# Optimization experiments

Hardware: AMD Instinct MI355X
Metric: run time of the kernel (lower is better)

The kernel has to match this reference:

```python
import jax, jax.numpy as jnp
import numpy as np

B, T, D, H = 4, 2048, 1024, 16
DH = D // H  # 64


def setup_inputs() -> dict:
    key = jax.random.key(0)
    ks = jax.random.split(key, 5)
    s = 0.02
    return {
        "x": jax.random.normal(ks[0], (B, T, D), dtype=jnp.float32),
        "Wq": jax.random.normal(ks[1], (D, D), dtype=jnp.float32) * s,
        "Wk": jax.random.normal(ks[2], (D, D), dtype=jnp.float32) * s,
        "Wv": jax.random.normal(ks[3], (D, D), dtype=jnp.float32) * s,
        "Wo": jax.random.normal(ks[4], (D, D), dtype=jnp.float32) * s,
        "bo": jnp.zeros((D,), dtype=jnp.float32),
    }


def reference(x, Wq, Wk, Wv, Wo, bo):
    b, t, d = x.shape
    # QKV projections (no bias, matching qkv_bias=False)
    q = (x @ Wq).reshape(b, t, H, DH).transpose(0, 2, 1, 3)  # [B,H,T,Dh]
    k = (x @ Wk).reshape(b, t, H, DH).transpose(0, 2, 1, 3)
    v = (x @ Wv).reshape(b, t, H, DH).transpose(0, 2, 1, 3)
    scores = jnp.einsum('bhqd,bhkd->bhqk', q, k)  # [B,H,T,T]
    # mask strictly-upper triangle (future positions) with -inf, then scale
    causal = jnp.triu(jnp.ones((t, t), dtype=bool), k=1)
    scores = jnp.where(causal[None, None], -jnp.inf, scores)
    attn = jax.nn.softmax(scores / np.float32(np.sqrt(DH)), axis=-1)
    ctx = jnp.einsum('bhqk,bhkd->bhqd', attn, v)  # [B,H,T,Dh]
    ctx = ctx.transpose(0, 2, 1, 3).reshape(b, t, d)
    return ctx @ Wo + bo
```

## Files before the change

kernel.cpp:

```cpp
#include <hip/hip_runtime.h>
#include <math.h>
#include <stdint.h>

typedef unsigned short u16;
typedef __bf16 bf16x8 __attribute__((ext_vector_type(8)));
typedef unsigned short u16x8 __attribute__((ext_vector_type(8)));
typedef float f32x4 __attribute__((ext_vector_type(4)));

constexpr int Tc = 2048, Dc = 1024, Hc = 16, Mc = 8192;
constexpr size_t NQKV = (size_t)Mc * Dc;
constexpr size_t NW = (size_t)Dc * Dc;

__device__ __forceinline__ u16 f2bf(float f) {
    union { float f; uint32_t u; } c; c.f = f;
    uint32_t u = c.u;
    u += 0x7FFFu + ((u >> 16) & 1u);
    return (u16)(u >> 16);
}

__device__ __forceinline__ bf16x8 ldbf8(const u16* p) {
    u16x8 v = *(const u16x8*)p;
    return __builtin_bit_cast(bf16x8, v);
}

__device__ __forceinline__ float fexp2(float x) {
#if __has_builtin(__builtin_amdgcn_exp2f)
    return __builtin_amdgcn_exp2f(x);
#else
    return exp2f(x);
#endif
}

__device__ __forceinline__ void gload_lds16(const void* g, void* l) {
    __builtin_amdgcn_global_load_lds(
        (__attribute__((address_space(1))) void*)(uintptr_t)g,
        (__attribute__((address_space(3))) void*)l, 16, 0, 0);
}

__global__ __launch_bounds__(256)
void cvt_x_kernel(const float* __restrict__ x, u16* __restrict__ xb)
{
    int i = blockIdx.x * 256 + threadIdx.x;
    float4 v = ((const float4*)x)[i];
    ushort4 o;
    o.x = f2bf(v.x); o.y = f2bf(v.y); o.z = f2bf(v.z); o.w = f2bf(v.w);
    ((ushort4*)xb)[i] = o;
}

__global__ __launch_bounds__(256)
void wt_cvt_kernel(const float* __restrict__ Wq, const float* __restrict__ Wk,
                   const float* __restrict__ Wv, const float* __restrict__ Wo,
                   u16* __restrict__ WTq, u16* __restrict__ WTk,
                   u16* __restrict__ WTv, u16* __restrict__ WTo)
{
    __shared__ float Ts[64][65];
    const int z = blockIdx.z;
    const float* W = (z == 0) ? Wq : (z == 1) ? Wk : (z == 2) ? Wv : Wo;
    u16* WT        = (z == 0) ? WTq : (z == 1) ? WTk : (z == 2) ? WTv : WTo;
    const int k0 = blockIdx.x * 64, n0 = blockIdx.y * 64;
    const int tid = threadIdx.x;
    #pragma unroll
    for (int it = 0; it < 16; ++it) {
        int flat = it * 256 + tid;
        int r = flat >> 6, c = flat & 63;
        Ts[r][c] = W[(size_t)(k0 + r) * Dc + n0 + c];
    }
    __syncthreads();
    #pragma unroll
    for (int it = 0; it < 16; ++it) {
        int flat = it * 256 + tid;
        int rn = flat >> 6, ck = flat & 63;
        WT[(size_t)(n0 + rn) * Dc + k0 + ck] = f2bf(Ts[ck][rn]);
    }
}

__global__ __launch_bounds__(256)
void qkv_gemm_kernel(const u16* __restrict__ xb,
                     const u16* __restrict__ WTq, const u16* __restrict__ WTk,
                     const u16* __restrict__ WTv,
                     u16* __restrict__ Qb, u16* __restrict__ Kb, u16* __restrict__ Vb)
{
    const int z = blockIdx.z;
    const u16* WT = (z == 0) ? WTq : (z == 1) ? WTk : WTv;
    u16* outp     = (z == 0) ? Qb  : (z == 1) ? Kb  : Vb;
    const float scale = (z == 0) ? 0.125f * 1.44269504088896f : 1.0f;

    __shared__ __align__(16) u16 As[128 * 32];
    __shared__ __align__(16) u16 Bs[128 * 32];

    const int tid = threadIdx.x, lane = tid & 63, w = tid >> 6;
    const int wm = w >> 1, wn = w & 1;
    const int m0 = blockIdx.x * 128, n0 = blockIdx.y * 128;

    f32x4 acc[4][4] = {};

    for (int k0 = 0; k0 < Dc; k0 += 32) {
        __syncthreads();
        #pragma unroll
        for (int t = 0; t < 2; ++t) {
            int ci = w * 64 + t * 256 + lane;
            int r = ci >> 2, p = ci & 3;
            int pc = p ^ ((r >> 1) & 3);
            gload_lds16(xb + (size_t)(m0 + r) * Dc + k0 + pc * 8,
                        As + (size_t)(w * 64 + t * 256) * 8);
            gload_lds16(WT + (size_t)(n0 + r) * Dc + k0 + pc * 8,
                        Bs + (size_t)(w * 64 + t * 256) * 8);
        }
        __syncthreads();

        bf16x8 a[4], b[4];
        #pragma unroll
        for (int i = 0; i < 4; ++i) {
            int row = wm * 64 + i * 16 + (lane & 15);
            a[i] = ldbf8(As + row * 32 + (((lane >> 4) ^ ((row >> 1) & 3)) * 8));
            int col = wn * 64 + i * 16 + (lane & 15);
            b[i] = ldbf8(Bs + col * 32 + (((lane >> 4) ^ ((col >> 1) & 3)) * 8));
        }
        #pragma unroll
        for (int i = 0; i < 4; ++i)
            #pragma unroll
            for (int j = 0; j < 4; ++j)
                acc[i][j] = __builtin_amdgcn_mfma_f32_16x16x32_bf16(a[i], b[j], acc[i][j], 0, 0, 0);
    }

    #pragma unroll
    for (int j = 0; j < 4; ++j) {
        int n = n0 + wn * 64 + j * 16 + (lane & 15);
        int hh = n >> 6, dh = n & 63;
        #pragma unroll
        for (int i = 0; i < 4; ++i) {
            #pragma unroll
            for (int r = 0; r < 4; ++r) {
                int m = m0 + wm * 64 + i * 16 + (lane >> 4) * 4 + r;
                int bb = m >> 11, t = m & 2047;
                outp[((size_t)(bb * Hc + hh) * Tc + t) * 64 + dh] = f2bf(acc[i][j][r] * scale);
            }
        }
    }
}

__global__ __launch_bounds__(256)
void v_transpose_kernel(const u16* __restrict__ Vb, u16* __restrict__ VTb)
{
    __shared__ u16 Ts[64][68];
    const int tid = threadIdx.x;
    const int bh = blockIdx.y, t0 = blockIdx.x * 64;
    const size_t vbase = (size_t)bh * Tc * 64;
    #pragma unroll
    for (int it = 0; it < 4; ++it) {
        int flat = it * 1024 + tid * 4;
        int r = flat >> 6, c = flat & 63;
        *(ushort4*)&Ts[r][c] = *(const ushort4*)(Vb + vbase + (size_t)(t0 + r) * 64 + c);
    }
    __syncthreads();
    const size_t obase = (size_t)bh * 64 * Tc;
    #pragma unroll
    for (int it = 0; it < 4; ++it) {
        int flat = it * 1024 + tid * 4;
        int d = flat >> 6, tl = flat & 63;
        ushort4 o;
        o.x = Ts[tl][d]; o.y = Ts[tl + 1][d]; o.z = Ts[tl + 2][d]; o.w = Ts[tl + 3][d];
        *(ushort4*)(VTb + obase + (size_t)d * Tc + t0 + tl) = o;
    }
}

__global__ __launch_bounds__(256)
void attn_mfma_kernel(const u16* __restrict__ Qb, const u16* __restrict__ Kb,
                      const u16* __restrict__ VTb, u16* __restrict__ ctxb)
{
    __shared__ __align__(16) u16 Ks[64 * 64];
    __shared__ __align__(16) u16 Vs[64 * 64];
    __shared__ __align__(16) u16 Ps[4][32 * 72];

    const int tid = threadIdx.x, lane = tid & 63, w = tid >> 6;
    const int g = lane >> 4, lq = lane & 15;
    const int p_idx = blockIdx.y & 7;
    const int bh = (blockIdx.x << 3) | (blockIdx.y >> 3);
    const size_t qkbase = (size_t)bh * Tc * 64;
    const size_t vtbase = (size_t)bh * 64 * Tc;
    const int b = bh >> 4, h = bh & 15;
    u16* pw = &Ps[w][0];

    #pragma unroll 1
    for (int pass = 0; pass < 2; ++pass) {
        const int qt = pass ? (15 - p_idx) : p_idx;
        const int q0 = qt * 128;
        const int nkt = qt * 2 + 2;

        bf16x8 qf[2][2];
        #pragma unroll
        for (int qfi = 0; qfi < 2; ++qfi)
            #pragma unroll
            for (int kf = 0; kf < 2; ++kf) {
                int row = q0 + w * 32 + qfi * 16 + lq;
                qf[qfi][kf] = ldbf8(Qb + qkbase + (size_t)row * 64 + kf * 32 + g * 8);
            }

        f32x4 o_acc[2][4] = {};
        float m_run[2] = {-INFINITY, -INFINITY};
        float l_run[2] = {0.f, 0.f};

        for (int kt = 0; kt < nkt; ++kt) {
            const int kv0 = kt * 64;
            __syncthreads();
            #pragma unroll
            for (int t = 0; t < 2; ++t) {
                int ci = w * 64 + t * 256 + lane;
                int r = ci >> 3, p = ci & 7;
                int pc = p ^ (r & 7);
                gload_lds16(Kb + qkbase + (size_t)(kv0 + r) * 64 + pc * 8,
                            Ks + (size_t)(w * 64 + t * 256) * 8);
                gload_lds16(VTb + vtbase + (size_t)r * Tc + kv0 + pc * 8,
                            Vs + (size_t)(w * 64 + t * 256) * 8);
            }
            __syncthreads();

            f32x4 s[4][2] = {};
            __builtin_amdgcn_s_setprio(1);
            #pragma unroll
            for (int kf = 0; kf < 2; ++kf) {
                bf16x8 kb[4];
                #pragma unroll
                for (int ni = 0; ni < 4; ++ni) {
                    int rr = ni * 16 + lq;
                    int pc = (g + 4 * kf) ^ (rr & 7);
                    kb[ni] = ldbf8(Ks + rr * 64 + pc * 8);
                }
                #pragma unroll
                for (int ni = 0; ni < 4; ++ni)
                    #pragma unroll
                    for (int qfi = 0; qfi < 2; ++qfi)
                        s[ni][qfi] = __builtin_amdgcn_mfma_f32_16x16x32_bf16(kb[ni], qf[qfi][kf], s[ni][qfi], 0, 0, 0);
            }
            __builtin_amdgcn_s_setprio(0);

            if (kt >= nkt - 2) {
                #pragma unroll
                for (int ni = 0; ni < 4; ++ni)
                    #pragma unroll
                    for (int qfi = 0; qfi < 2; ++qfi)
                        #pragma unroll
                        for (int r = 0; r < 4; ++r) {
                            int kv = kv0 + ni * 16 + 4 * g + r;
                            int q  = q0 + w * 32 + qfi * 16 + lq;
                            if (kv > q) s[ni][qfi][r] = -INFINITY;
                        }
            }

            #pragma unroll
            for (int qfi = 0; qfi < 2; ++qfi) {
                float mrow = -INFINITY;
                #pragma unroll
                for (int ni = 0; ni < 4; ++ni)
                    #pragma unroll
                    for (int r = 0; r < 4; ++r) mrow = fmaxf(mrow, s[ni][qfi][r]);
                mrow = fmaxf(mrow, __shfl_xor(mrow, 16, 64));
                mrow = fmaxf(mrow, __shfl_xor(mrow, 32, 64));
                if (!__all(mrow <= m_run[qfi] + 12.0f)) {
                    float mnew  = fmaxf(m_run[qfi], mrow);
                    float alpha = fexp2(m_run[qfi] - mnew);
                    m_run[qfi] = mnew;
                    l_run[qfi] *= alpha;
                    #pragma unroll
                    for (int r = 0; r < 4; ++r) {
                        float ar = __shfl(alpha, 4 * g + r, 16);
                        #pragma unroll
                        for (int nd = 0; nd < 4; ++nd) o_acc[qfi][nd][r] *= ar;
                    }
                }
                float mq = m_run[qfi];
                float sum = 0.f;
                #pragma unroll
                for (int ni = 0; ni < 4; ++ni)
                    #pragma unroll
                    for (int r = 0; r < 4; ++r) {
                        float pe = fexp2(s[ni][qfi][r] - mq);
                        s[ni][qfi][r] = pe;
                        sum += pe;
                    }
                sum += __shfl_xor(sum, 16, 64);
                sum += __shfl_xor(sum, 32, 64);
                l_run[qfi] += sum;
            }

            #pragma unroll
            for (int qfi = 0; qfi < 2; ++qfi)
                #pragma unroll
                for (int ni = 0; ni < 4; ++ni) {
                    float a0 = s[ni][qfi][0], a1 = s[ni][qfi][1];
                    float a2 = s[ni][qfi][2], a3 = s[ni][qfi][3];
                    uint32_t lo, hi;
                    asm volatile("v_cvt_pk_bf16_f32 %0, %1, %2" : "=v"(lo) : "v"(a0), "v"(a1));
                    asm volatile("v_cvt_pk_bf16_f32 %0, %1, %2" : "=v"(hi) : "v"(a2), "v"(a3));
                    uint2 pk = make_uint2(lo, hi);
                    *(uint2*)(pw + (qfi * 16 + lq) * 72 + ni * 16 + 4 * g) = pk;
                }

            bf16x8 pa[2][2];
            #pragma unroll
            for (int qfi = 0; qfi < 2; ++qfi)
                #pragma unroll
                for (int kf = 0; kf < 2; ++kf)
                    pa[qfi][kf] = ldbf8(pw + (qfi * 16 + lq) * 72 + kf * 32 + 8 * g);
            __builtin_amdgcn_s_setprio(1);
            #pragma unroll
            for (int kf = 0; kf < 2; ++kf) {
                bf16x8 vb[4];
                #pragma unroll
                for (int nd = 0; nd < 4; ++nd) {
                    int rr = nd * 16 + lq;
                    int pc = (g + 4 * kf) ^ (rr & 7);
                    vb[nd] = ldbf8(Vs + rr * 64 + pc * 8);
                }
                #pragma unroll
                for (int qfi = 0; qfi < 2; ++qfi)
                    #pragma unroll
                    for (int nd = 0; nd < 4; ++nd)
                        o_acc[qfi][nd] = __builtin_amdgcn_mfma_f32_16x16x32_bf16(pa[qfi][kf], vb[nd], o_acc[qfi][nd], 0, 0, 0);
            }
            __builtin_amdgcn_s_setprio(0);
        }

        #pragma unroll
        for (int qfi = 0; qfi < 2; ++qfi)
            #pragma unroll
            for (int r = 0; r < 4; ++r) {
                float lr = __shfl(l_run[qfi], 4 * g + r, 16);
                float inv = 1.0f / lr;
                int qrow = q0 + w * 32 + qfi * 16 + 4 * g + r;
                #pragma unroll
                for (int nd = 0; nd < 4; ++nd) {
                    int d = h * 64 + nd * 16 + lq;
                    ctxb[(size_t)(b * Tc + qrow) * Dc + d] = f2bf(o_acc[qfi][nd][r] * inv);
                }
            }
    }
}

__global__ __launch_bounds__(256)
void out_gemm_kernel(const u16* __restrict__ ctxb, const u16* __restrict__ WTo,
                     const float* __restrict__ bo, float* __restrict__ out)
{
    __shared__ __align__(16) u16 As[128 * 32];
    __shared__ __align__(16) u16 Bs[128 * 32];

    const int tid = threadIdx.x, lane = tid & 63, w = tid >> 6;
    const int wm = w >> 1, wn = w & 1;
    const int m0 = blockIdx.x * 128, n0 = blockIdx.y * 128;

    f32x4 acc[4][4] = {};

    for (int k0 = 0; k0 < Dc; k0 += 32) {
        __syncthreads();
        #pragma unroll
        for (int t = 0; t < 2; ++t) {
            int ci = w * 64 + t * 256 + lane;
            int r = ci >> 2, p = ci & 3;
            int pc = p ^ ((r >> 1) & 3);
            gload_lds16(ctxb + (size_t)(m0 + r) * Dc + k0 + pc * 8,
                        As + (size_t)(w * 64 + t * 256) * 8);
            gload_lds16(WTo + (size_t)(n0 + r) * Dc + k0 + pc * 8,
                        Bs + (size_t)(w * 64 + t * 256) * 8);
        }
        __syncthreads();

        bf16x8 a[4], b[4];
        #pragma unroll
        for (int i = 0; i < 4; ++i) {
            int row = wm * 64 + i * 16 + (lane & 15);
            a[i] = ldbf8(As + row * 32 + (((lane >> 4) ^ ((row >> 1) & 3)) * 8));
            int col = wn * 64 + i * 16 + (lane & 15);
            b[i] = ldbf8(Bs + col * 32 + (((lane >> 4) ^ ((col >> 1) & 3)) * 8));
        }
        #pragma unroll
        for (int i = 0; i < 4; ++i)
            #pragma unroll
            for (int j = 0; j < 4; ++j)
                acc[i][j] = __builtin_amdgcn_mfma_f32_16x16x32_bf16(a[i], b[j], acc[i][j], 0, 0, 0);
    }

    #pragma unroll
    for (int j = 0; j < 4; ++j) {
        int n = n0 + wn * 64 + j * 16 + (lane & 15);
        float bias = bo[n];
        #pragma unroll
        for (int i = 0; i < 4; ++i) {
            #pragma unroll
            for (int r = 0; r < 4; ++r) {
                int m = m0 + wm * 64 + i * 16 + (lane >> 4) * 4 + r;
                out[(size_t)m * Dc + n] = acc[i][j][r] + bias;
            }
        }
    }
}

extern "C" void kernel_launch(void* const* d_in, const int* in_sizes, int n_in,
                              void* d_out, int out_size, void* d_ws, size_t ws_size,
                              hipStream_t stream)
{
    const float* x  = (const float*)d_in[0];
    const float* Wq = (const float*)d_in[1];
    const float* Wk = (const float*)d_in[2];
    const float* Wv = (const float*)d_in[3];
    const float* Wo = (const float*)d_in[4];
    const float* bo = (const float*)d_in[5];
    float* out = (float*)d_out;

    u16* xb   = (u16*)d_ws;
    u16* WTq  = xb + NQKV;
    u16* WTk  = WTq + NW;
    u16* WTv  = WTk + NW;
    u16* WTo  = WTv + NW;
    u16* Qb   = WTo + NW;
    u16* Kb   = Qb + NQKV;
    u16* Vb   = Kb + NQKV;
    u16* VTb  = Vb + NQKV;
    u16* ctxb = VTb + NQKV;

    cvt_x_kernel<<<8192, 256, 0, stream>>>(x, xb);
    wt_cvt_kernel<<<dim3(16, 16, 4), 256, 0, stream>>>(Wq, Wk, Wv, Wo, WTq, WTk, WTv, WTo);
    qkv_gemm_kernel<<<dim3(64, 8, 3), 256, 0, stream>>>(xb, WTq, WTk, WTv, Qb, Kb, Vb);
    v_transpose_kernel<<<dim3(32, 64), 256, 0, stream>>>(Vb, VTb);
    attn_mfma_kernel<<<dim3(8, 64), 256, 0, stream>>>(Qb, Kb, VTb, ctxb);
    out_gemm_kernel<<<dim3(64, 8), 256, 0, stream>>>(ctxb, WTo, bo, out);
}
```

Before: 257.8 us.

## Load K/V fragments directly from global per wave and drop shared-memory staging

The attention kernel no longer stages K and V^T tiles cooperatively in LDS behind block-wide barriers. Each wave now loads its MFMA operands straight from global memory (relying on L1/L2 for reuse) and iterates only over the KV tiles its own 32 query rows need. This removes the two __syncthreads per tile and lets waves skip fully masked tiles independently. In exchange, each wave repeats the global loads that the block previously shared, and the loads are 16-byte per lane with no swizzle.

```diff
diff --git a/kernel.cpp b/kernel.cpp
--- a/kernel.cpp
+++ b/kernel.cpp
@@ -168,8 +168,6 @@
 void attn_mfma_kernel(const u16* __restrict__ Qb, const u16* __restrict__ Kb,
                       const u16* __restrict__ VTb, u16* __restrict__ ctxb)
 {
-    __shared__ __align__(16) u16 Ks[64 * 64];
-    __shared__ __align__(16) u16 Vs[64 * 64];
     __shared__ __align__(16) u16 Ps[4][32 * 72];
 
     const int tid = threadIdx.x, lane = tid & 63, w = tid >> 6;
@@ -184,15 +182,15 @@
     #pragma unroll 1
     for (int pass = 0; pass < 2; ++pass) {
         const int qt = pass ? (15 - p_idx) : p_idx;
-        const int q0 = qt * 128;
-        const int nkt = qt * 2 + 2;
+        const int q0 = qt * 128 + w * 32;
+        const int nkt = (q0 >> 6) + 1;
 
         bf16x8 qf[2][2];
         #pragma unroll
         for (int qfi = 0; qfi < 2; ++qfi)
             #pragma unroll
             for (int kf = 0; kf < 2; ++kf) {
-                int row = q0 + w * 32 + qfi * 16 + lq;
+                int row = q0 + qfi * 16 + lq;
                 qf[qfi][kf] = ldbf8(Qb + qkbase + (size_t)row * 64 + kf * 32 + g * 8);
             }
 
@@ -200,41 +198,27 @@
         float m_run[2] = {-INFINITY, -INFINITY};
         float l_run[2] = {0.f, 0.f};
 
+        #pragma unroll 1
         for (int kt = 0; kt < nkt; ++kt) {
             const int kv0 = kt * 64;
-            __syncthreads();
-            #pragma unroll
-            for (int t = 0; t < 2; ++t) {
-                int ci = w * 64 + t * 256 + lane;
-                int r = ci >> 3, p = ci & 7;
-                int pc = p ^ (r & 7);
-                gload_lds16(Kb + qkbase + (size_t)(kv0 + r) * 64 + pc * 8,
-                            Ks + (size_t)(w * 64 + t * 256) * 8);
-                gload_lds16(VTb + vtbase + (size_t)r * Tc + kv0 + pc * 8,
-                            Vs + (size_t)(w * 64 + t * 256) * 8);
-            }
-            __syncthreads();
 
             f32x4 s[4][2] = {};
-            __builtin_amdgcn_s_setprio(1);
             #pragma unroll
             for (int kf = 0; kf < 2; ++kf) {
                 bf16x8 kb[4];
                 #pragma unroll
-                for (int ni = 0; ni < 4; ++ni) {
-                    int rr = ni * 16 + lq;
-                    int pc = (g + 4 * kf) ^ (rr & 7);
-                    kb[ni] = ldbf8(Ks + rr * 64 + pc * 8);
-                }
+                for (int ni = 0; ni < 4; ++ni)
+                    kb[ni] = ldbf8(Kb + qkbase + (size_t)(kv0 + ni * 16 + lq) * 64 + kf * 32 + g * 8);
+                __builtin_amdgcn_s_setprio(1);
                 #pragma unroll
                 for (int ni = 0; ni < 4; ++ni)
                     #pragma unroll
                     for (int qfi = 0; qfi < 2; ++qfi)
                         s[ni][qfi] = __builtin_amdgcn_mfma_f32_16x16x32_bf16(kb[ni], qf[qfi][kf], s[ni][qfi], 0, 0, 0);
-            }
-            __builtin_amdgcn_s_setprio(0);
-
-            if (kt >= nkt - 2) {
+                __builtin_amdgcn_s_setprio(0);
+            }
+
+            if (kt == nkt - 1) {
                 #pragma unroll
                 for (int ni = 0; ni < 4; ++ni)
                     #pragma unroll
@@ -242,7 +226,7 @@
                         #pragma unroll
                         for (int r = 0; r < 4; ++r) {
                             int kv = kv0 + ni * 16 + 4 * g + r;
-                            int q  = q0 + w * 32 + qfi * 16 + lq;
+                            int q  = q0 + qfi * 16 + lq;
                             if (kv > q) s[ni][qfi][r] = -INFINITY;
                         }
             }
@@ -302,23 +286,20 @@
                 #pragma unroll
                 for (int kf = 0; kf < 2; ++kf)
                     pa[qfi][kf] = ldbf8(pw + (qfi * 16 + lq) * 72 + kf * 32 + 8 * g);
-            __builtin_amdgcn_s_setprio(1);
             #pragma unroll
             for (int kf = 0; kf < 2; ++kf) {
                 bf16x8 vb[4];
                 #pragma unroll
-                for (int nd = 0; nd < 4; ++nd) {
-                    int rr = nd * 16 + lq;
-                    int pc = (g + 4 * kf) ^ (rr & 7);
-                    vb[nd] = ldbf8(Vs + rr * 64 + pc * 8);
-                }
+                for (int nd = 0; nd < 4; ++nd)
+                    vb[nd] = ldbf8(VTb + vtbase + (size_t)(nd * 16 + lq) * Tc + kv0 + kf * 32 + g * 8);
+                __builtin_amdgcn_s_setprio(1);
                 #pragma unroll
                 for (int qfi = 0; qfi < 2; ++qfi)
                     #pragma unroll
                     for (int nd = 0; nd < 4; ++nd)
                         o_acc[qfi][nd] = __builtin_amdgcn_mfma_f32_16x16x32_bf16(pa[qfi][kf], vb[nd], o_acc[qfi][nd], 0, 0, 0);
-            }
-            __builtin_amdgcn_s_setprio(0);
+                __builtin_amdgcn_s_setprio(0);
+            }
         }
 
         #pragma unroll
@@ -327,7 +308,7 @@
             for (int r = 0; r < 4; ++r) {
                 float lr = __shfl(l_run[qfi], 4 * g + r, 16);
                 float inv = 1.0f / lr;
-                int qrow = q0 + w * 32 + qfi * 16 + 4 * g + r;
+                int qrow = q0 + qfi * 16 + 4 * g + r;
                 #pragma unroll
                 for (int nd = 0; nd < 4; ++nd) {
                     int d = h * 64 + nd * 16 + lq;
```

New measurement: 311.8 us. 1.21x slower.
